# Performance work log

Hardware: AMD Instinct MI355X
Metric: run time of the kernel (lower is better)

## Reference

```python
import jax, jax.numpy as jnp
import numpy as np

N_SRC = 50000
N_DST = 50000
E = 800000
D = 128
K = 8  # args.k: number of randomly sampled neighbors


def setup_inputs() -> dict:
    key = jax.random.key(0)
    k1, k2, k3, k4, k5, k6 = jax.random.split(key, 6)
    h_src = jax.random.normal(k1, (N_SRC, D), dtype=jnp.float32)
    h_dst = jax.random.normal(k2, (N_DST, D), dtype=jnp.float32)
    unif = jax.random.uniform(k3, (N_DST, K), dtype=jnp.float32)
    src_idx = jax.random.randint(k4, (E,), 0, N_SRC, dtype=jnp.int32)
    dst_idx = jnp.sort(jax.random.randint(k5, (E,), 0, N_DST, dtype=jnp.int32))
    category = jax.random.randint(k6, (N_SRC,), 0, 50, dtype=jnp.int32)
    return {"h_src": h_src, "h_dst": h_dst, "unif": unif,
            "src_idx": src_idx, "dst_idx": dst_idx, "category": category}


def _forward(h_src, h_dst, unif, src_idx, dst_idx, category):
    n_src = h_src.shape[0]
    n_dst = h_dst.shape[0]
    e = src_idx.shape[0]
    ones = jnp.ones((e,), dtype=h_src.dtype)

    # src-side symmetric norm: feat_src * out_deg^-0.5
    out_deg = jax.ops.segment_sum(ones, src_idx, num_segments=n_src)
    out_norm = jnp.clip(out_deg, 1.0, None) ** -0.5
    feat_src = h_src * out_norm[:, None]

    # mailbox gather: message per edge m_e = feat_src[src_e]  -> [E, D]
    msg = feat_src[src_idx]

    # in-degrees and full segment-sum reduction
    in_deg = jax.ops.segment_sum(ones, dst_idx, num_segments=n_dst)
    full_sum = jax.ops.segment_sum(msg, dst_idx, num_segments=n_dst)  # [N_dst, D]

    # random neighbor subsampling with replacement (dst_idx is sorted):
    # node n owns edges [ptr[n], ptr[n]+deg[n]); pick K offsets via floor(u*deg)
    deg_i = in_deg.astype(jnp.int32)
    ptr = jnp.searchsorted(dst_idx, jnp.arange(n_dst, dtype=jnp.int32), side="left").astype(jnp.int32)
    off = jnp.floor(unif * in_deg[:, None]).astype(jnp.int32)
    off = jnp.minimum(off, jnp.maximum(deg_i[:, None] - 1, 0))  # guard u==1 / deg==0
    eid = jnp.clip(ptr[:, None] + off, 0, e - 1)                # [N_dst, K]
    samp_sum = msg[eid].sum(axis=1)                              # [N_dst, D]

    # bucket escape hatch: any incoming category == -1 -> sum everything
    neg_in = jax.ops.segment_sum((category[src_idx] == -1).astype(jnp.int32),
                                 dst_idx, num_segments=n_dst)
    use_full = (deg_i <= K) | (neg_in > 0)
    rst = jnp.where(use_full[:, None], full_sum, samp_sum)

    # dst-side norm: rst * in_deg^-0.5
    in_norm = jnp.clip(in_deg, 1.0, None) ** -0.5
    return rst * in_norm[:, None]


def reference(h_src, h_dst, unif, src_idx, dst_idx, category):
    return _forward(h_src, h_dst, unif, src_idx, dst_idx, category)
```

## Files before the change

### kernel.cpp

```cpp
#include <hip/hip_runtime.h>

#define N_SRC 50000
#define N_DST 50000
#define E_CNT 800000
#define D 128
#define K 8

#define HIST_BLOCKS 64
#define HIST_THREADS 512
#define PTR_BLOCKS ((N_DST + 1 + HIST_THREADS - 1) / HIST_THREADS)
#define HALF 25000
#define HWORDS (HALF / 2)
#define NCHUNK (E_CNT / 4)


__device__ __forceinline__ int lower_bound_dst(const int* __restrict__ d, int key) {
    int lo = 0, hi = E_CNT;
    while (lo < hi) {
        int mid = (lo + hi) >> 1;
        if (d[mid] < key) lo = mid + 1; else hi = mid;
    }
    return lo;
}

__global__ __launch_bounds__(HIST_THREADS)
void count_ptr_kernel(const int* __restrict__ src_idx,
                      const int* __restrict__ dst_idx,
                      const int* __restrict__ category,
                      const float* __restrict__ unif,
                      int* __restrict__ slab,
                      int* __restrict__ neg_in,
                      int* __restrict__ ptr,
                      float* __restrict__ in_norm,
                      int* __restrict__ samp,
                      unsigned char* __restrict__ degs) {
    if (blockIdx.x < HIST_BLOCKS) {
        __shared__ int hist[HWORDS];
        const int4* s4 = (const int4*)src_idx;
        int* myslab = slab + (size_t)blockIdx.x * N_SRC;

        for (int pass = 0; pass < 2; ++pass) {
            int base = pass * HALF;
            for (int j = threadIdx.x; j < HWORDS; j += HIST_THREADS) hist[j] = 0;
            __syncthreads();

            for (int c = blockIdx.x * HIST_THREADS + threadIdx.x; c < NCHUNK;
                 c += HIST_BLOCKS * HIST_THREADS) {
                int4 s = s4[c];
                int r;
                r = s.x - base; if ((unsigned)r < HALF) atomicAdd(&hist[r >> 1], 1 << ((r & 1) * 16));
                r = s.y - base; if ((unsigned)r < HALF) atomicAdd(&hist[r >> 1], 1 << ((r & 1) * 16));
                r = s.z - base; if ((unsigned)r < HALF) atomicAdd(&hist[r >> 1], 1 << ((r & 1) * 16));
                r = s.w - base; if ((unsigned)r < HALF) atomicAdd(&hist[r >> 1], 1 << ((r & 1) * 16));
                if (pass == 0) {
                    if (category[s.x] == -1) atomicAdd(&neg_in[dst_idx[4 * c + 0]], 1);
                    if (category[s.y] == -1) atomicAdd(&neg_in[dst_idx[4 * c + 1]], 1);
                    if (category[s.z] == -1) atomicAdd(&neg_in[dst_idx[4 * c + 2]], 1);
                    if (category[s.w] == -1) atomicAdd(&neg_in[dst_idx[4 * c + 3]], 1);
                }
            }
            __syncthreads();

            for (int j = threadIdx.x; j < HWORDS; j += HIST_THREADS) {
                unsigned w = (unsigned)hist[j];
                ((int2*)(myslab + base))[j] = make_int2((int)(w & 0xffffu), (int)(w >> 16));
            }
            __syncthreads();
        }
    } else {
        int n = (blockIdx.x - HIST_BLOCKS) * HIST_THREADS + threadIdx.x;
        int lane = threadIdx.x & 63;
        int lo = 0;
        if (n <= N_DST) {
            lo = lower_bound_dst(dst_idx, n);
            ptr[n] = lo;
        }
        int hi = __shfl_down(lo, 1, 64);
        if (lane == 63 && n < N_DST) hi = lower_bound_dst(dst_idx, n + 1);
        if (n >= N_DST) return;

        int deg = hi - lo;
        in_norm[n] = rsqrtf((float)max(deg, 1));
        int m = min(deg, K);
        degs[n] = (unsigned char)m;

        int ids[K];
        if (deg > K) {
            const float4* u4 = (const float4*)(unif + (size_t)n * K);
            float4 ua = u4[0], ub = u4[1];
            float uu[K] = {ua.x, ua.y, ua.z, ua.w, ub.x, ub.y, ub.z, ub.w};
            #pragma unroll
            for (int k = 0; k < K; ++k) {
                int off = (int)floorf(uu[k] * (float)deg);
                if (off > deg - 1) off = deg - 1;
                if (off < 0) off = 0;
                int eid = lo + off;
                if (eid > E_CNT - 1) eid = E_CNT - 1;
                ids[k] = src_idx[eid];
            }
        } else {
            #pragma unroll
            for (int k = 0; k < K; ++k) {
                int eid = lo + k;
                if (eid > E_CNT - 1) eid = E_CNT - 1;
                ids[k] = src_idx[eid];
            }
        }
        int4* sp = (int4*)(samp + (size_t)n * K);
        sp[0] = make_int4(ids[0], ids[1], ids[2], ids[3]);
        sp[1] = make_int4(ids[4], ids[5], ids[6], ids[7]);
    }
}

__global__ void reduce_norm_kernel(const int* __restrict__ slab,
                                   float* __restrict__ out_norm) {
    int n = blockIdx.x * blockDim.x + threadIdx.x;
    if (n >= N_SRC) return;
    int d = 0;
    #pragma unroll
    for (int b = 0; b < HIST_BLOCKS; ++b) d += slab[(size_t)b * N_SRC + n];
    out_norm[n] = rsqrtf((float)max(d, 1));
}

__global__ void gather_kernel(const float* __restrict__ h_src,
                              const int* __restrict__ src_idx,
                              const float* __restrict__ out_norm,
                              const int* __restrict__ neg_in,
                              const int* __restrict__ ptr,
                              const float* __restrict__ in_norm,
                              const int* __restrict__ samp,
                              const unsigned char* __restrict__ degs,
                              float* __restrict__ out) {
    int wave = (blockIdx.x * blockDim.x + threadIdx.x) >> 6;
    int lane = threadIdx.x & 63;
    int sub = lane & 31;
    int hbase = lane & 32;
    int n = wave * 2 + (lane >> 5);
    if (n >= N_DST) return;

    int neg = neg_in[n];
    int m = degs[n];
    float inr = in_norm[n];

    const float4* h4 = (const float4*)h_src;
    float4 acc = make_float4(0.f, 0.f, 0.f, 0.f);

    if (neg > 0) {
        int p = ptr[n];
        int deg = ptr[n + 1] - p;
        for (int i = 0; i < deg; ++i) {
            int s = src_idx[p + i];
            float nrm = out_norm[s];
            float4 v = h4[(size_t)s * 32 + sub];
            acc.x += v.x * nrm;
            acc.y += v.y * nrm;
            acc.z += v.z * nrm;
            acc.w += v.w * nrm;
        }
    } else {
        int s_k = 0;
        float n_k = 0.f;
        if (sub < K) {
            s_k = samp[(size_t)n * K + sub];
            n_k = (sub < m) ? out_norm[s_k] : 0.f;
        }
        #pragma unroll
        for (int k = 0; k < K; ++k) {
            int s = __shfl(s_k, hbase + k, 64);
            float nrm = __shfl(n_k, hbase + k, 64);
            float4 v = h4[(size_t)s * 32 + sub];
            acc.x += v.x * nrm;
            acc.y += v.y * nrm;
            acc.z += v.z * nrm;
            acc.w += v.w * nrm;
        }
    }

    float4 r;
    r.x = acc.x * inr;
    r.y = acc.y * inr;
    r.z = acc.z * inr;
    r.w = acc.w * inr;
    ((float4*)out)[(size_t)n * 32 + sub] = r;
}

extern "C" void kernel_launch(void* const* d_in, const int* in_sizes, int n_in,
                              void* d_out, int out_size, void* d_ws, size_t ws_size,
                              hipStream_t stream) {
    const float* h_src   = (const float*)d_in[0];
    const float* unif    = (const float*)d_in[2];
    const int* src_idx   = (const int*)d_in[3];
    const int* dst_idx   = (const int*)d_in[4];
    const int* category  = (const int*)d_in[5];
    float* out = (float*)d_out;

    int* slab      = (int*)d_ws;
    int* neg_in    = slab + (size_t)HIST_BLOCKS * N_SRC;
    int* ptr       = neg_in + N_DST;
    float* out_norm = (float*)(ptr + N_DST + 4);
    float* in_norm  = out_norm + N_SRC;
    int* samp      = (int*)(in_norm + N_DST);
    unsigned char* degs = (unsigned char*)(samp + (size_t)N_DST * K);

    hipMemsetAsync(neg_in, 0, (size_t)N_DST * sizeof(int), stream);

    count_ptr_kernel<<<HIST_BLOCKS + PTR_BLOCKS, HIST_THREADS, 0, stream>>>(
        src_idx, dst_idx, category, unif, slab, neg_in, ptr, in_norm, samp, degs);

    reduce_norm_kernel<<<(N_SRC + 255) / 256, 256, 0, stream>>>(slab, out_norm);

    {
        int threads = 256;
        int blocks = (N_DST + 7) / 8;
        gather_kernel<<<blocks, threads, 0, stream>>>(h_src, src_idx, out_norm,
                                                      neg_in, ptr, in_norm,
                                                      samp, degs, out);
    }
}
```

Baseline: 139.2 us.

## Replace per-node negative-category atomics with global flag; pack histogram slabs

Drops the per-edge neg_in global atomics and the memset, keeping only one per-block flag reduced into a single any_neg word. The gather kernel then rescans a node's edges for category -1 only when that flag is set. The per-block histogram is now stored as packed 16-bit pairs, halving slab traffic, and the histogram block count doubles. The cost is extra scan work in the gather whenever any -1 category exists, while the test data (categories 0..49) never takes that path.

```diff
diff --git a/kernel.cpp b/kernel.cpp
--- a/kernel.cpp
+++ b/kernel.cpp
@@ -6,11 +6,12 @@
 #define D 128
 #define K 8
 
-#define HIST_BLOCKS 64
+#define HIST_BLOCKS 128
 #define HIST_THREADS 512
 #define PTR_BLOCKS ((N_DST + 1 + HIST_THREADS - 1) / HIST_THREADS)
 #define HALF 25000
 #define HWORDS (HALF / 2)
+#define SLAB_WORDS (N_SRC / 2)
 #define NCHUNK (E_CNT / 4)
 
 
@@ -28,16 +29,19 @@
                       const int* __restrict__ dst_idx,
                       const int* __restrict__ category,
                       const float* __restrict__ unif,
-                      int* __restrict__ slab,
-                      int* __restrict__ neg_in,
+                      unsigned* __restrict__ slab,
+                      int* __restrict__ blockflag,
                       int* __restrict__ ptr,
                       float* __restrict__ in_norm,
                       int* __restrict__ samp,
                       unsigned char* __restrict__ degs) {
     if (blockIdx.x < HIST_BLOCKS) {
-        __shared__ int hist[HWORDS];
+        __shared__ unsigned hist[HWORDS];
+        __shared__ int blkneg;
+        if (threadIdx.x == 0) blkneg = 0;
         const int4* s4 = (const int4*)src_idx;
-        int* myslab = slab + (size_t)blockIdx.x * N_SRC;
+        unsigned* myslab = slab + (size_t)blockIdx.x * SLAB_WORDS;
+        int negf = 0;
 
         for (int pass = 0; pass < 2; ++pass) {
             int base = pass * HALF;
@@ -48,25 +52,24 @@
                  c += HIST_BLOCKS * HIST_THREADS) {
                 int4 s = s4[c];
                 int r;
-                r = s.x - base; if ((unsigned)r < HALF) atomicAdd(&hist[r >> 1], 1 << ((r & 1) * 16));
-                r = s.y - base; if ((unsigned)r < HALF) atomicAdd(&hist[r >> 1], 1 << ((r & 1) * 16));
-                r = s.z - base; if ((unsigned)r < HALF) atomicAdd(&hist[r >> 1], 1 << ((r & 1) * 16));
-                r = s.w - base; if ((unsigned)r < HALF) atomicAdd(&hist[r >> 1], 1 << ((r & 1) * 16));
+                r = s.x - base; if ((unsigned)r < HALF) atomicAdd(&hist[r >> 1], 1u << ((r & 1) * 16));
+                r = s.y - base; if ((unsigned)r < HALF) atomicAdd(&hist[r >> 1], 1u << ((r & 1) * 16));
+                r = s.z - base; if ((unsigned)r < HALF) atomicAdd(&hist[r >> 1], 1u << ((r & 1) * 16));
+                r = s.w - base; if ((unsigned)r < HALF) atomicAdd(&hist[r >> 1], 1u << ((r & 1) * 16));
                 if (pass == 0) {
-                    if (category[s.x] == -1) atomicAdd(&neg_in[dst_idx[4 * c + 0]], 1);
-                    if (category[s.y] == -1) atomicAdd(&neg_in[dst_idx[4 * c + 1]], 1);
-                    if (category[s.z] == -1) atomicAdd(&neg_in[dst_idx[4 * c + 2]], 1);
-                    if (category[s.w] == -1) atomicAdd(&neg_in[dst_idx[4 * c + 3]], 1);
+                    negf |= (category[s.x] == -1) | (category[s.y] == -1) |
+                            (category[s.z] == -1) | (category[s.w] == -1);
                 }
             }
             __syncthreads();
 
-            for (int j = threadIdx.x; j < HWORDS; j += HIST_THREADS) {
-                unsigned w = (unsigned)hist[j];
-                ((int2*)(myslab + base))[j] = make_int2((int)(w & 0xffffu), (int)(w >> 16));
-            }
+            for (int j = threadIdx.x; j < HWORDS; j += HIST_THREADS)
+                myslab[pass * HWORDS + j] = hist[j];
             __syncthreads();
         }
+        if (negf) atomicOr(&blkneg, 1);
+        __syncthreads();
+        if (threadIdx.x == 0) blockflag[blockIdx.x] = blkneg;
     } else {
         int n = (blockIdx.x - HIST_BLOCKS) * HIST_THREADS + threadIdx.x;
         int lane = threadIdx.x & 63;
@@ -112,20 +115,37 @@
     }
 }
 
-__global__ void reduce_norm_kernel(const int* __restrict__ slab,
-                                   float* __restrict__ out_norm) {
-    int n = blockIdx.x * blockDim.x + threadIdx.x;
-    if (n >= N_SRC) return;
-    int d = 0;
-    #pragma unroll
-    for (int b = 0; b < HIST_BLOCKS; ++b) d += slab[(size_t)b * N_SRC + n];
-    out_norm[n] = rsqrtf((float)max(d, 1));
+__global__ __launch_bounds__(256)
+void reduce_norm_kernel(const unsigned* __restrict__ slab,
+                        const int* __restrict__ blockflag,
+                        float* __restrict__ out_norm,
+                        int* __restrict__ any_neg) {
+    int w = blockIdx.x * 256 + threadIdx.x;
+    if (blockIdx.x == 0 && threadIdx.x == 0) {
+        int f = 0;
+        #pragma unroll 16
+        for (int b = 0; b < HIST_BLOCKS; ++b) f |= blockflag[b];
+        *any_neg = f;
+    }
+    if (w >= SLAB_WORDS) return;
+    int lo = 0, hi = 0;
+    #pragma unroll 16
+    for (int b = 0; b < HIST_BLOCKS; ++b) {
+        unsigned v = slab[(size_t)b * SLAB_WORDS + w];
+        lo += (int)(v & 0xffffu);
+        hi += (int)(v >> 16);
+    }
+    int pass = w / HWORDS;
+    int j = w - pass * HWORDS;
+    float2 r = make_float2(rsqrtf((float)max(lo, 1)), rsqrtf((float)max(hi, 1)));
+    ((float2*)out_norm)[pass * HWORDS + j] = r;
 }
 
 __global__ void gather_kernel(const float* __restrict__ h_src,
                               const int* __restrict__ src_idx,
+                              const int* __restrict__ category,
                               const float* __restrict__ out_norm,
-                              const int* __restrict__ neg_in,
+                              const int* __restrict__ any_neg,
                               const int* __restrict__ ptr,
                               const float* __restrict__ in_norm,
                               const int* __restrict__ samp,
@@ -138,26 +158,34 @@
     int n = wave * 2 + (lane >> 5);
     if (n >= N_DST) return;
 
-    int neg = neg_in[n];
     int m = degs[n];
     float inr = in_norm[n];
 
     const float4* h4 = (const float4*)h_src;
     float4 acc = make_float4(0.f, 0.f, 0.f, 0.f);
 
-    if (neg > 0) {
+    bool escape = false;
+    if (*any_neg) {
         int p = ptr[n];
         int deg = ptr[n + 1] - p;
-        for (int i = 0; i < deg; ++i) {
-            int s = src_idx[p + i];
-            float nrm = out_norm[s];
-            float4 v = h4[(size_t)s * 32 + sub];
-            acc.x += v.x * nrm;
-            acc.y += v.y * nrm;
-            acc.z += v.z * nrm;
-            acc.w += v.w * nrm;
-        }
-    } else {
+        for (int i = 0; i < deg && !escape; ++i)
+            escape = (category[src_idx[p + i]] == -1);
+        if (escape && deg > K) {
+            for (int i = 0; i < deg; ++i) {
+                int s = src_idx[p + i];
+                float nrm = out_norm[s];
+                float4 v = h4[(size_t)s * 32 + sub];
+                acc.x += v.x * nrm;
+                acc.y += v.y * nrm;
+                acc.z += v.z * nrm;
+                acc.w += v.w * nrm;
+            }
+        } else {
+            escape = false;
+        }
+    }
+
+    if (!escape) {
         int s_k = 0;
         float n_k = 0.f;
         if (sub < K) {
@@ -194,26 +222,27 @@
     const int* category  = (const int*)d_in[5];
     float* out = (float*)d_out;
 
-    int* slab      = (int*)d_ws;
-    int* neg_in    = slab + (size_t)HIST_BLOCKS * N_SRC;
-    int* ptr       = neg_in + N_DST;
+    unsigned* slab  = (unsigned*)d_ws;
+    int* blockflag  = (int*)(slab + (size_t)HIST_BLOCKS * SLAB_WORDS);
+    int* any_neg    = blockflag + HIST_BLOCKS;
+    int* ptr        = any_neg + 4;
     float* out_norm = (float*)(ptr + N_DST + 4);
     float* in_norm  = out_norm + N_SRC;
-    int* samp      = (int*)(in_norm + N_DST);
+    int* samp       = (int*)(in_norm + N_DST);
     unsigned char* degs = (unsigned char*)(samp + (size_t)N_DST * K);
 
-    hipMemsetAsync(neg_in, 0, (size_t)N_DST * sizeof(int), stream);
 
     count_ptr_kernel<<<HIST_BLOCKS + PTR_BLOCKS, HIST_THREADS, 0, stream>>>(
-        src_idx, dst_idx, category, unif, slab, neg_in, ptr, in_norm, samp, degs);
-
-    reduce_norm_kernel<<<(N_SRC + 255) / 256, 256, 0, stream>>>(slab, out_norm);
+        src_idx, dst_idx, category, unif, slab, blockflag, ptr, in_norm, samp, degs);
+
+    reduce_norm_kernel<<<(SLAB_WORDS + 255) / 256, 256, 0, stream>>>(
+        slab, blockflag, out_norm, any_neg);
 
     {
         int threads = 256;
         int blocks = (N_DST + 7) / 8;
-        gather_kernel<<<blocks, threads, 0, stream>>>(h_src, src_idx, out_norm,
-                                                      neg_in, ptr, in_norm,
-                                                      samp, degs, out);
-    }
-}
+        gather_kernel<<<blocks, threads, 0, stream>>>(h_src, src_idx, category,
+                                                      out_norm, any_neg, ptr,
+                                                      in_norm, samp, degs, out);
+    }
+}
```

Measured after the change: 134.1 us. 1.04x faster.
